# Kernel optimization log

Hardware: AMD Instinct MI355X
Metric: run time of the kernel (lower is better)

The kernel has to match this reference:

```python
import jax, jax.numpy as jnp
import numpy as np

D = 128  # feature_dim

def setup_inputs() -> dict:
    key = jax.random.key(0)
    ks = jax.random.split(key, 10)
    B, Sq, Skv = 32, 2048, 2048
    scale = 1.0 / np.sqrt(D)
    inp = {
        'smiles_features': jax.random.normal(ks[0], (B, Skv, D), jnp.float32),
        'image_features': jax.random.normal(ks[1], (B, Sq, D), jnp.float32),
        'Wv': jax.random.normal(ks[2], (D, D), jnp.float32) * scale,
        'bv': jnp.zeros((D,), jnp.float32),
        'Wk': jax.random.normal(ks[3], (D, D), jnp.float32) * scale,
        'bk': jnp.zeros((D,), jnp.float32),
        'Wq': jax.random.normal(ks[4], (D, D), jnp.float32) * scale,
        'bq': jnp.zeros((D,), jnp.float32),
        'Wd': jax.random.normal(ks[5], (D, D), jnp.float32) * scale,
        'bd': jnp.zeros((D,), jnp.float32),
    }
    return inp

def reference(smiles_features, image_features, Wv, bv, Wk, bk, Wq, bq, Wd, bd):
    # Linear layers: y = x @ W^T + b (torch convention)
    V = smiles_features @ Wv.T + bv          # [B, Skv, D]
    K = smiles_features @ Wk.T + bk          # [B, Skv, D]
    Q = image_features @ Wq.T + bq           # [B, Sq, D]
    # energy = Q K^T / sqrt(128) (hard-coded 128 in original)
    energy = jnp.einsum('bqd,bkd->bqk', Q, K) / jnp.sqrt(jnp.float32(128.0))
    attention = jax.nn.softmax(energy, axis=-1)
    fusion = jnp.einsum('bqk,bkd->bqd', attention, V)
    output = fusion @ Wd.T + bd
    return output
```

## Files before the change

### kernel.cpp

```cpp
#include <hip/hip_runtime.h>
#include <hip/hip_bf16.h>

typedef __attribute__((ext_vector_type(4))) float f32x4;
typedef __attribute__((ext_vector_type(16))) float f32x16;
typedef __attribute__((ext_vector_type(8))) short bf16x8;
typedef __attribute__((ext_vector_type(4))) unsigned int uint4v;
typedef __attribute__((ext_vector_type(2))) unsigned int uint2v;

#define MFMA16(a, b, c) __builtin_amdgcn_mfma_f32_16x16x32_bf16(a, b, c, 0, 0, 0)
#define MFMA32(a, b, c) __builtin_amdgcn_mfma_f32_32x32x16_bf16(a, b, c, 0, 0, 0)

__device__ __forceinline__ unsigned short f2bf(float f) {
  union { float f; unsigned u; } v; v.f = f;
  unsigned r = v.u + 0x7fffu + ((v.u >> 16) & 1u);
  return (unsigned short)(r >> 16);
}
__device__ __forceinline__ unsigned pack2(float a, float b) {
  union { __hip_bfloat162 h2; unsigned u; } cv;
  cv.h2 = __hip_bfloat162(__float2bfloat16(a), __float2bfloat16(b));
  return cv.u;
}

__device__ __forceinline__ void swap32(unsigned a, unsigned b, int hi,
                                       unsigned& ox, unsigned& oy) {
#if __has_builtin(__builtin_amdgcn_permlane32_swap)
  uint2v r = __builtin_amdgcn_permlane32_swap(a, b, false, false);
  ox = r[0]; oy = r[1];
#else
  unsigned sb = __shfl_xor(b, 32);
  unsigned sa = __shfl_xor(a, 32);
  ox = hi ? sb : a;
  oy = hi ? b : sa;
#endif
}

template<bool IN_F32, int OUT_MODE>
__global__ __launch_bounds__(256)
void proj_kernel(const void* __restrict__ xin, const float* __restrict__ W,
                 const float* __restrict__ bias, void* __restrict__ yout,
                 float scale)
{
  __shared__ __align__(16) unsigned short Ws[128][136];
  __shared__ __align__(16) unsigned short Xs[64][136];
  const int t = threadIdx.x;
  const int wid = t >> 6;
  const int lane = t & 63;
  const int ln = lane & 15, g = lane >> 4;
  const long row0 = (long)blockIdx.x * 64;

  float bz[8];
#pragma unroll
  for (int tt = 0; tt < 8; ++tt) bz[tt] = bias[tt * 16 + ln];

#pragma unroll
  for (int i = 0; i < 16; ++i) {
    int idx = (i * 256 + t) * 4;
    int r = idx >> 7, c = idx & 127;
    const float4 w4 = *reinterpret_cast<const float4*>(W + idx);
    ushort4 wb;
    wb.x = f2bf(w4.x); wb.y = f2bf(w4.y); wb.z = f2bf(w4.z); wb.w = f2bf(w4.w);
    *reinterpret_cast<ushort4*>(&Ws[r][c]) = wb;
  }
  if (IN_F32) {
    const float* x = (const float*)xin;
#pragma unroll
    for (int i = 0; i < 8; ++i) {
      int idx = (i * 256 + t) * 4;
      int r = idx >> 7, c = idx & 127;
      const float4 x4 = *reinterpret_cast<const float4*>(x + row0 * 128 + idx);
      ushort4 xb;
      xb.x = f2bf(x4.x); xb.y = f2bf(x4.y); xb.z = f2bf(x4.z); xb.w = f2bf(x4.w);
      *reinterpret_cast<ushort4*>(&Xs[r][c]) = xb;
    }
  } else {
    const unsigned short* x = (const unsigned short*)xin;
#pragma unroll
    for (int i = 0; i < 4; ++i) {
      int idx = (i * 256 + t) * 8;
      int r = idx >> 7, c = idx & 127;
      *reinterpret_cast<uint4v*>(&Xs[r][c]) =
          *reinterpret_cast<const uint4v*>(x + row0 * 128 + idx);
    }
  }
  __syncthreads();

  f32x4 acc[8];
#pragma unroll
  for (int tt = 0; tt < 8; ++tt) acc[tt] = (f32x4){0.f, 0.f, 0.f, 0.f};

#pragma unroll
  for (int c = 0; c < 4; ++c) {
    bf16x8 af = *reinterpret_cast<const bf16x8*>(&Xs[wid * 16 + ln][c * 32 + g * 8]);
#pragma unroll
    for (int tt = 0; tt < 8; ++tt) {
      bf16x8 bfr = *reinterpret_cast<const bf16x8*>(&Ws[tt * 16 + ln][c * 32 + g * 8]);
      acc[tt] = MFMA16(af, bfr, acc[tt]);
    }
  }

#pragma unroll
  for (int tt = 0; tt < 8; ++tt) {
#pragma unroll
    for (int r = 0; r < 4; ++r) {
      long row = row0 + wid * 16 + g * 4 + r;
      int col = tt * 16 + ln;
      float val = (acc[tt][r] + bz[tt]) * scale;
      if (OUT_MODE == 2) {
        ((float*)yout)[row * 128 + col] = val;
      } else if (OUT_MODE == 0) {
        ((unsigned short*)yout)[row * 128 + col] = f2bf(val);
      } else {
        long bb = row >> 11, rr = row & 2047;
        ((unsigned short*)yout)[(bb * 128 + col) * 2048 + rr] = f2bf(val);
      }
    }
  }
}

__global__ __launch_bounds__(256)
void proj_kv_kernel(const float* __restrict__ x,
                    const float* __restrict__ Wk, const float* __restrict__ bk,
                    const float* __restrict__ Wv, const float* __restrict__ bv,
                    unsigned short* __restrict__ Kout,
                    unsigned short* __restrict__ Vout)
{
  __shared__ __align__(16) unsigned short Ws[128][136];
  __shared__ __align__(16) unsigned short Xs[64][136];
  const int t = threadIdx.x;
  const int wid = t >> 6;
  const int lane = t & 63;
  const int ln = lane & 15, g = lane >> 4;
  const long row0 = (long)blockIdx.x * 64;

  float bzk[8], bzv[8];
#pragma unroll
  for (int tt = 0; tt < 8; ++tt) { bzk[tt] = bk[tt * 16 + ln]; bzv[tt] = bv[tt * 16 + ln]; }

#pragma unroll
  for (int i = 0; i < 8; ++i) {
    int idx = (i * 256 + t) * 4;
    int r = idx >> 7, c = idx & 127;
    const float4 x4 = *reinterpret_cast<const float4*>(x + row0 * 128 + idx);
    ushort4 xb;
    xb.x = f2bf(x4.x); xb.y = f2bf(x4.y); xb.z = f2bf(x4.z); xb.w = f2bf(x4.w);
    *reinterpret_cast<ushort4*>(&Xs[r][c]) = xb;
  }
#pragma unroll
  for (int i = 0; i < 16; ++i) {
    int idx = (i * 256 + t) * 4;
    int r = idx >> 7, c = idx & 127;
    const float4 w4 = *reinterpret_cast<const float4*>(Wk + idx);
    ushort4 wb;
    wb.x = f2bf(w4.x); wb.y = f2bf(w4.y); wb.z = f2bf(w4.z); wb.w = f2bf(w4.w);
    *reinterpret_cast<ushort4*>(&Ws[r][c]) = wb;
  }
  __syncthreads();

  f32x4 acc[8];
#pragma unroll
  for (int tt = 0; tt < 8; ++tt) acc[tt] = (f32x4){0.f, 0.f, 0.f, 0.f};
#pragma unroll
  for (int c = 0; c < 4; ++c) {
    bf16x8 af = *reinterpret_cast<const bf16x8*>(&Xs[wid * 16 + ln][c * 32 + g * 8]);
#pragma unroll
    for (int tt = 0; tt < 8; ++tt) {
      bf16x8 bfr = *reinterpret_cast<const bf16x8*>(&Ws[tt * 16 + ln][c * 32 + g * 8]);
      acc[tt] = MFMA16(af, bfr, acc[tt]);
    }
  }
#pragma unroll
  for (int tt = 0; tt < 8; ++tt)
#pragma unroll
    for (int r = 0; r < 4; ++r) {
      long row = row0 + wid * 16 + g * 4 + r;
      Kout[row * 128 + tt * 16 + ln] = f2bf(acc[tt][r] + bzk[tt]);
    }

  __syncthreads();
#pragma unroll
  for (int i = 0; i < 16; ++i) {
    int idx = (i * 256 + t) * 4;
    int r = idx >> 7, c = idx & 127;
    const float4 w4 = *reinterpret_cast<const float4*>(Wv + idx);
    ushort4 wb;
    wb.x = f2bf(w4.x); wb.y = f2bf(w4.y); wb.z = f2bf(w4.z); wb.w = f2bf(w4.w);
    *reinterpret_cast<ushort4*>(&Ws[r][c]) = wb;
  }
  __syncthreads();

#pragma unroll
  for (int tt = 0; tt < 8; ++tt) acc[tt] = (f32x4){0.f, 0.f, 0.f, 0.f};
#pragma unroll
  for (int c = 0; c < 4; ++c) {
    bf16x8 af = *reinterpret_cast<const bf16x8*>(&Xs[wid * 16 + ln][c * 32 + g * 8]);
#pragma unroll
    for (int tt = 0; tt < 8; ++tt) {
      bf16x8 bfr = *reinterpret_cast<const bf16x8*>(&Ws[tt * 16 + ln][c * 32 + g * 8]);
      acc[tt] = MFMA16(af, bfr, acc[tt]);
    }
  }
#pragma unroll
  for (int tt = 0; tt < 8; ++tt)
#pragma unroll
    for (int r = 0; r < 4; ++r) {
      long row = row0 + wid * 16 + g * 4 + r;
      long bb = row >> 11, rr = row & 2047;
      Vout[(bb * 128 + tt * 16 + ln) * 2048 + rr] = f2bf(acc[tt][r] + bzv[tt]);
    }
}

__global__ __launch_bounds__(256)
void attn_kernel(const unsigned short* __restrict__ Qg,
                 const unsigned short* __restrict__ Kg,
                 const unsigned short* __restrict__ Vtg,
                 unsigned short* __restrict__ Fg)
{
  __shared__ __align__(16) unsigned short Ks[32][136];
  __shared__ __align__(16) unsigned short Vs[128][40];

  const int t = threadIdx.x;
  const int lane = t & 63;
  const int q = lane & 31;
  const int hi = lane >> 5;
  const int wid = t >> 6;

  const int gbid = blockIdx.x;
  const int k_ = gbid >> 3, r_ = gbid & 7;
  const int b = r_ + 8 * (k_ >> 4);
  const int j = k_ & 15;
  const int q0 = j * 128 + wid * 32;

  const unsigned short* Qb = Qg + (long)b * 2048 * 128;
  const unsigned short* Kb = Kg + (long)b * 2048 * 128;
  const unsigned short* Vb = Vtg + (long)b * 128 * 2048;

  const int kr = t >> 4, kc = (t & 15) * 8;
  const int vc = t >> 2, ko = (t & 3) * 8;

  bf16x8 qf[8];
#pragma unroll
  for (int c = 0; c < 8; ++c)
    qf[c] = *reinterpret_cast<const bf16x8*>(
        Qb + (long)(q0 + q) * 128 + c * 16 + hi * 8);

  f32x16 o[4];
#pragma unroll
  for (int dc = 0; dc < 4; ++dc)
#pragma unroll
    for (int r = 0; r < 16; ++r) o[dc][r] = 0.f;
  float mrun = -1e30f;
  float lrun = 0.f;

  uint4v kreg0 = *reinterpret_cast<const uint4v*>(Kb + (long)kr * 128 + kc);
  uint4v kreg1 = *reinterpret_cast<const uint4v*>(Kb + (long)(kr + 16) * 128 + kc);
  uint4v vreg0 = *reinterpret_cast<const uint4v*>(Vb + (long)vc * 2048 + ko);
  uint4v vreg1 = *reinterpret_cast<const uint4v*>(Vb + (long)(vc + 64) * 2048 + ko);

  for (int kt = 0; kt < 64; ++kt) {
    __syncthreads();
    *reinterpret_cast<uint4v*>(&Ks[kr][kc]) = kreg0;
    *reinterpret_cast<uint4v*>(&Ks[kr + 16][kc]) = kreg1;
    *reinterpret_cast<uint4v*>(&Vs[vc][ko]) = vreg0;
    *reinterpret_cast<uint4v*>(&Vs[vc + 64][ko]) = vreg1;
    __syncthreads();

    if (kt < 63) {
      const int nv0 = (kt + 1) * 32;
      kreg0 = *reinterpret_cast<const uint4v*>(Kb + (long)(nv0 + kr) * 128 + kc);
      kreg1 = *reinterpret_cast<const uint4v*>(Kb + (long)(nv0 + kr + 16) * 128 + kc);
      vreg0 = *reinterpret_cast<const uint4v*>(Vb + (long)vc * 2048 + nv0 + ko);
      vreg1 = *reinterpret_cast<const uint4v*>(Vb + (long)(vc + 64) * 2048 + nv0 + ko);
    }

    f32x16 st;
#pragma unroll
    for (int r = 0; r < 16; ++r) st[r] = 0.f;
    __builtin_amdgcn_s_setprio(1);
#pragma unroll
    for (int c = 0; c < 8; ++c) {
      bf16x8 kf = *reinterpret_cast<const bf16x8*>(&Ks[q][c * 16 + hi * 8]);
      st = MFMA32(kf, qf[c], st);
    }
    __builtin_amdgcn_s_setprio(0);

    float tm = st[0];
#pragma unroll
    for (int r = 1; r < 16; ++r) tm = fmaxf(tm, st[r]);
    tm = fmaxf(tm, __shfl_xor(tm, 32));

    float mcur = mrun;
    if (!__all(tm <= mcur + 8.0f)) {
      float mnew = fmaxf(mcur, tm);
      float al = __builtin_amdgcn_exp2f(mcur - mnew);
      mrun = mnew;
      mcur = mnew;
      lrun *= al;
#pragma unroll
      for (int r = 0; r < 16; ++r) {
        float ar = __shfl(al, (r & 3) + 8 * (r >> 2) + 4 * hi);
#pragma unroll
        for (int dc = 0; dc < 4; ++dc) o[dc][r] *= ar;
      }
    }

    unsigned pk[8];
    float s[8];
#pragma unroll
    for (int j2 = 0; j2 < 8; ++j2) {
      float pa_ = __builtin_amdgcn_exp2f(st[2 * j2] - mcur);
      float pb_ = __builtin_amdgcn_exp2f(st[2 * j2 + 1] - mcur);
      s[j2] = pa_ + pb_;
      pk[j2] = pack2(pa_, pb_);
    }
#pragma unroll
    for (int j2 = 0; j2 < 4; ++j2) s[j2] += s[j2 + 4];
    lrun += (s[0] + s[1]) + (s[2] + s[3]);

    union { unsigned u[4]; bf16x8 v; } pa0, pa1;
    swap32(pk[0], pk[2], hi, pa0.u[0], pa0.u[2]);
    swap32(pk[1], pk[3], hi, pa0.u[1], pa0.u[3]);
    swap32(pk[4], pk[6], hi, pa1.u[0], pa1.u[2]);
    swap32(pk[5], pk[7], hi, pa1.u[1], pa1.u[3]);

    __builtin_amdgcn_s_setprio(1);
#pragma unroll
    for (int dc = 0; dc < 4; ++dc) {
      bf16x8 vf0 = *reinterpret_cast<const bf16x8*>(&Vs[dc * 32 + q][hi * 8]);
      bf16x8 vf1 = *reinterpret_cast<const bf16x8*>(&Vs[dc * 32 + q][16 + hi * 8]);
      o[dc] = MFMA32(pa0.v, vf0, o[dc]);
      o[dc] = MFMA32(pa1.v, vf1, o[dc]);
    }
    __builtin_amdgcn_s_setprio(0);
  }

  float ltot = lrun + __shfl_xor(lrun, 32);
  float inv = 1.f / ltot;
#pragma unroll
  for (int r = 0; r < 16; ++r) {
    const int qr = (r & 3) + 8 * (r >> 2) + 4 * hi;
    float invr = __shfl(inv, qr);
    long row = (long)b * 2048 + q0 + qr;
#pragma unroll
    for (int dc = 0; dc < 4; ++dc)
      Fg[row * 128 + dc * 32 + q] = f2bf(o[dc][r] * invr);
  }
}

extern "C" void kernel_launch(void* const* d_in, const int* in_sizes, int n_in,
                              void* d_out, int out_size, void* d_ws, size_t ws_size,
                              hipStream_t stream)
{
  (void)in_sizes; (void)n_in; (void)out_size; (void)ws_size;
  const float* smiles = (const float*)d_in[0];
  const float* image  = (const float*)d_in[1];
  const float* Wv = (const float*)d_in[2]; const float* bv = (const float*)d_in[3];
  const float* Wk = (const float*)d_in[4]; const float* bk = (const float*)d_in[5];
  const float* Wq = (const float*)d_in[6]; const float* bq = (const float*)d_in[7];
  const float* Wd = (const float*)d_in[8]; const float* bd = (const float*)d_in[9];

  unsigned short* Qw = (unsigned short*)d_ws;
  unsigned short* Kw = Qw + 8388608;
  unsigned short* Vw = Kw + 8388608;
  unsigned short* Fw = Vw + 8388608;

  const float qscale = 1.4426950408889634f * 0.08838834764831845f;

  dim3 blk(256);
  proj_kernel<true, 0><<<dim3(1024), blk, 0, stream>>>(image, Wq, bq, Qw, qscale);
  proj_kv_kernel<<<dim3(1024), blk, 0, stream>>>(smiles, Wk, bk, Wv, bv, Kw, Vw);
  attn_kernel<<<dim3(512), blk, 0, stream>>>(Qw, Kw, Vw, Fw);
  proj_kernel<false, 2><<<dim3(1024), blk, 0, stream>>>(Fw, Wd, bd, (float*)d_out, 1.f);
}
```

Measured before the change: 128.1 us.

## Process two 32-row query tiles per wave to reuse K/V LDS fragments

Each wave now handles 64 query rows (two 32-row tiles) instead of 32, so every K and V fragment read from shared memory feeds two MFMAs and each block covers 256 query rows. The grid shrinks from 512 to 256 blocks, halving the global K/V tile traffic per query and the sync overhead per unit of work. The cost is roughly doubled accumulator and Q register usage, which may lower occupancy. With only 256 blocks, the grid may also underfill the GPU's 256 CUs.

```diff
diff --git a/kernel.cpp b/kernel.cpp
--- a/kernel.cpp
+++ b/kernel.cpp
@@ -226,9 +226,9 @@
 
   const int gbid = blockIdx.x;
   const int k_ = gbid >> 3, r_ = gbid & 7;
-  const int b = r_ + 8 * (k_ >> 4);
-  const int j = k_ & 15;
-  const int q0 = j * 128 + wid * 32;
+  const int b = r_ + 8 * (k_ >> 3);
+  const int j = k_ & 7;
+  const int q0 = j * 256 + wid * 64;
 
   const unsigned short* Qb = Qg + (long)b * 2048 * 128;
   const unsigned short* Kb = Kg + (long)b * 2048 * 128;
@@ -237,19 +237,60 @@
   const int kr = t >> 4, kc = (t & 15) * 8;
   const int vc = t >> 2, ko = (t & 3) * 8;
 
-  bf16x8 qf[8];
-#pragma unroll
-  for (int c = 0; c < 8; ++c)
-    qf[c] = *reinterpret_cast<const bf16x8*>(
+  bf16x8 qf0[8], qf1[8];
+#pragma unroll
+  for (int c = 0; c < 8; ++c) {
+    qf0[c] = *reinterpret_cast<const bf16x8*>(
         Qb + (long)(q0 + q) * 128 + c * 16 + hi * 8);
-
-  f32x16 o[4];
+    qf1[c] = *reinterpret_cast<const bf16x8*>(
+        Qb + (long)(q0 + 32 + q) * 128 + c * 16 + hi * 8);
+  }
+
+  f32x16 o0[4], o1[4];
 #pragma unroll
   for (int dc = 0; dc < 4; ++dc)
 #pragma unroll
-    for (int r = 0; r < 16; ++r) o[dc][r] = 0.f;
-  float mrun = -1e30f;
-  float lrun = 0.f;
+    for (int r = 0; r < 16; ++r) { o0[dc][r] = 0.f; o1[dc][r] = 0.f; }
+  float mrun0 = -1e30f, mrun1 = -1e30f;
+  float lrun0 = 0.f, lrun1 = 0.f;
+
+  auto softmax_fn = [&](const f32x16& st, float& mr, float& lr, f32x16* oacc,
+                        bf16x8& pav0, bf16x8& pav1) {
+    float tm = st[0];
+#pragma unroll
+    for (int r = 1; r < 16; ++r) tm = fmaxf(tm, st[r]);
+    tm = fmaxf(tm, __shfl_xor(tm, 32));
+    float mcur = mr;
+    if (!__all(tm <= mcur + 8.0f)) {
+      float mnew = fmaxf(mcur, tm);
+      float al = __builtin_amdgcn_exp2f(mcur - mnew);
+      mr = mnew; mcur = mnew; lr *= al;
+#pragma unroll
+      for (int r = 0; r < 16; ++r) {
+        float ar = __shfl(al, (r & 3) + 8 * (r >> 2) + 4 * hi);
+#pragma unroll
+        for (int dc = 0; dc < 4; ++dc) oacc[dc][r] *= ar;
+      }
+    }
+    unsigned pk[8];
+    float s[8];
+#pragma unroll
+    for (int j2 = 0; j2 < 8; ++j2) {
+      float pa_ = __builtin_amdgcn_exp2f(st[2 * j2] - mcur);
+      float pb_ = __builtin_amdgcn_exp2f(st[2 * j2 + 1] - mcur);
+      s[j2] = pa_ + pb_;
+      pk[j2] = pack2(pa_, pb_);
+    }
+#pragma unroll
+    for (int j2 = 0; j2 < 4; ++j2) s[j2] += s[j2 + 4];
+    lr += (s[0] + s[1]) + (s[2] + s[3]);
+    union { unsigned u[4]; bf16x8 v; } A, B;
+    swap32(pk[0], pk[2], hi, A.u[0], A.u[2]);
+    swap32(pk[1], pk[3], hi, A.u[1], A.u[3]);
+    swap32(pk[4], pk[6], hi, B.u[0], B.u[2]);
+    swap32(pk[5], pk[7], hi, B.u[1], B.u[3]);
+    pav0 = A.v; pav1 = B.v;
+  };
 
   uint4v kreg0 = *reinterpret_cast<const uint4v*>(Kb + (long)kr * 128 + kc);
   uint4v kreg1 = *reinterpret_cast<const uint4v*>(Kb + (long)(kr + 16) * 128 + kc);
@@ -272,77 +313,60 @@
       vreg1 = *reinterpret_cast<const uint4v*>(Vb + (long)(vc + 64) * 2048 + nv0 + ko);
     }
 
-    f32x16 st;
-#pragma unroll
-    for (int r = 0; r < 16; ++r) st[r] = 0.f;
+    f32x16 st0, st1;
+#pragma unroll
+    for (int r = 0; r < 16; ++r) { st0[r] = 0.f; st1[r] = 0.f; }
     __builtin_amdgcn_s_setprio(1);
 #pragma unroll
     for (int c = 0; c < 8; ++c) {
       bf16x8 kf = *reinterpret_cast<const bf16x8*>(&Ks[q][c * 16 + hi * 8]);
-      st = MFMA32(kf, qf[c], st);
+      st0 = MFMA32(kf, qf0[c], st0);
+      st1 = MFMA32(kf, qf1[c], st1);
     }
     __builtin_amdgcn_s_setprio(0);
 
-    float tm = st[0];
-#pragma unroll
-    for (int r = 1; r < 16; ++r) tm = fmaxf(tm, st[r]);
-    tm = fmaxf(tm, __shfl_xor(tm, 32));
-
-    float mcur = mrun;
-    if (!__all(tm <= mcur + 8.0f)) {
-      float mnew = fmaxf(mcur, tm);
-      float al = __builtin_amdgcn_exp2f(mcur - mnew);
-      mrun = mnew;
-      mcur = mnew;
-      lrun *= al;
-#pragma unroll
-      for (int r = 0; r < 16; ++r) {
-        float ar = __shfl(al, (r & 3) + 8 * (r >> 2) + 4 * hi);
-#pragma unroll
-        for (int dc = 0; dc < 4; ++dc) o[dc][r] *= ar;
-      }
-    }
-
-    unsigned pk[8];
-    float s[8];
-#pragma unroll
-    for (int j2 = 0; j2 < 8; ++j2) {
-      float pa_ = __builtin_amdgcn_exp2f(st[2 * j2] - mcur);
-      float pb_ = __builtin_amdgcn_exp2f(st[2 * j2 + 1] - mcur);
-      s[j2] = pa_ + pb_;
-      pk[j2] = pack2(pa_, pb_);
-    }
-#pragma unroll
-    for (int j2 = 0; j2 < 4; ++j2) s[j2] += s[j2 + 4];
-    lrun += (s[0] + s[1]) + (s[2] + s[3]);
-
-    union { unsigned u[4]; bf16x8 v; } pa0, pa1;
-    swap32(pk[0], pk[2], hi, pa0.u[0], pa0.u[2]);
-    swap32(pk[1], pk[3], hi, pa0.u[1], pa0.u[3]);
-    swap32(pk[4], pk[6], hi, pa1.u[0], pa1.u[2]);
-    swap32(pk[5], pk[7], hi, pa1.u[1], pa1.u[3]);
+    bf16x8 paA0, paA1, paB0, paB1;
+    softmax_fn(st0, mrun0, lrun0, o0, paA0, paA1);
+    softmax_fn(st1, mrun1, lrun1, o1, paB0, paB1);
 
     __builtin_amdgcn_s_setprio(1);
 #pragma unroll
     for (int dc = 0; dc < 4; ++dc) {
       bf16x8 vf0 = *reinterpret_cast<const bf16x8*>(&Vs[dc * 32 + q][hi * 8]);
       bf16x8 vf1 = *reinterpret_cast<const bf16x8*>(&Vs[dc * 32 + q][16 + hi * 8]);
-      o[dc] = MFMA32(pa0.v, vf0, o[dc]);
-      o[dc] = MFMA32(pa1.v, vf1, o[dc]);
+      o0[dc] = MFMA32(paA0, vf0, o0[dc]);
+      o0[dc] = MFMA32(paA1, vf1, o0[dc]);
+      o1[dc] = MFMA32(paB0, vf0, o1[dc]);
+      o1[dc] = MFMA32(paB1, vf1, o1[dc]);
     }
     __builtin_amdgcn_s_setprio(0);
   }
 
-  float ltot = lrun + __shfl_xor(lrun, 32);
-  float inv = 1.f / ltot;
-#pragma unroll
-  for (int r = 0; r < 16; ++r) {
-    const int qr = (r & 3) + 8 * (r >> 2) + 4 * hi;
-    float invr = __shfl(inv, qr);
-    long row = (long)b * 2048 + q0 + qr;
-#pragma unroll
-    for (int dc = 0; dc < 4; ++dc)
-      Fg[row * 128 + dc * 32 + q] = f2bf(o[dc][r] * invr);
+  {
+    float ltot = lrun0 + __shfl_xor(lrun0, 32);
+    float inv = 1.f / ltot;
+#pragma unroll
+    for (int r = 0; r < 16; ++r) {
+      const int qr = (r & 3) + 8 * (r >> 2) + 4 * hi;
+      float invr = __shfl(inv, qr);
+      long row = (long)b * 2048 + q0 + qr;
+#pragma unroll
+      for (int dc = 0; dc < 4; ++dc)
+        Fg[row * 128 + dc * 32 + q] = f2bf(o0[dc][r] * invr);
+    }
+  }
+  {
+    float ltot = lrun1 + __shfl_xor(lrun1, 32);
+    float inv = 1.f / ltot;
+#pragma unroll
+    for (int r = 0; r < 16; ++r) {
+      const int qr = (r & 3) + 8 * (r >> 2) + 4 * hi;
+      float invr = __shfl(inv, qr);
+      long row = (long)b * 2048 + q0 + 32 + qr;
+#pragma unroll
+      for (int dc = 0; dc < 4; ++dc)
+        Fg[row * 128 + dc * 32 + q] = f2bf(o1[dc][r] * invr);
+    }
   }
 }
 
@@ -368,6 +392,6 @@
   dim3 blk(256);
   proj_kernel<true, 0><<<dim3(1024), blk, 0, stream>>>(image, Wq, bq, Qw, qscale);
   proj_kv_kernel<<<dim3(1024), blk, 0, stream>>>(smiles, Wk, bk, Wv, bv, Kw, Vw);
-  attn_kernel<<<dim3(512), blk, 0, stream>>>(Qw, Kw, Vw, Fw);
+  attn_kernel<<<dim3(256), blk, 0, stream>>>(Qw, Kw, Vw, Fw);
   proj_kernel<false, 2><<<dim3(1024), blk, 0, stream>>>(Fw, Wd, bd, (float*)d_out, 1.f);
 }
```

After: 170.2 us. +32.9%, slower.

## Merge Q/KV projections into one launch and double-buffer attention K/V tiles

Applied to the files above, without the earlier changes.

The Q projection and the K/V projection become one kernel with 2048 blocks, where the block index selects Q or K/V work. This removes one launch and lets both run concurrently on the GPU. The attention kernel now double-buffers its K and V shared-memory tiles, keeping one barrier per iteration instead of two and prefetching two tiles ahead. The cost is more LDS per block, which could lower occupancy, and uneven work between Q blocks and KV blocks in the merged launch.

```diff
diff --git a/kernel.cpp b/kernel.cpp
--- a/kernel.cpp
+++ b/kernel.cpp
@@ -107,22 +107,23 @@
       float val = (acc[tt][r] + bz[tt]) * scale;
       if (OUT_MODE == 2) {
         ((float*)yout)[row * 128 + col] = val;
-      } else if (OUT_MODE == 0) {
+      } else {
         ((unsigned short*)yout)[row * 128 + col] = f2bf(val);
-      } else {
-        long bb = row >> 11, rr = row & 2047;
-        ((unsigned short*)yout)[(bb * 128 + col) * 2048 + rr] = f2bf(val);
       }
     }
   }
 }
 
 __global__ __launch_bounds__(256)
-void proj_kv_kernel(const float* __restrict__ x,
-                    const float* __restrict__ Wk, const float* __restrict__ bk,
-                    const float* __restrict__ Wv, const float* __restrict__ bv,
-                    unsigned short* __restrict__ Kout,
-                    unsigned short* __restrict__ Vout)
+void proj_qkv_kernel(const float* __restrict__ image,
+                     const float* __restrict__ Wq, const float* __restrict__ bq,
+                     float qscale,
+                     const float* __restrict__ smiles,
+                     const float* __restrict__ Wk, const float* __restrict__ bk,
+                     const float* __restrict__ Wv, const float* __restrict__ bv,
+                     unsigned short* __restrict__ Qout,
+                     unsigned short* __restrict__ Kout,
+                     unsigned short* __restrict__ Vout)
 {
   __shared__ __align__(16) unsigned short Ws[128][136];
   __shared__ __align__(16) unsigned short Xs[64][136];
@@ -130,11 +131,9 @@
   const int wid = t >> 6;
   const int lane = t & 63;
   const int ln = lane & 15, g = lane >> 4;
-  const long row0 = (long)blockIdx.x * 64;
-
-  float bzk[8], bzv[8];
-#pragma unroll
-  for (int tt = 0; tt < 8; ++tt) { bzk[tt] = bk[tt * 16 + ln]; bzv[tt] = bv[tt * 16 + ln]; }
+  const bool isQ = blockIdx.x < 1024;
+  const long row0 = (long)(isQ ? blockIdx.x : blockIdx.x - 1024) * 64;
+  const float* x = isQ ? image : smiles;
 
 #pragma unroll
   for (int i = 0; i < 8; ++i) {
@@ -145,11 +144,18 @@
     xb.x = f2bf(x4.x); xb.y = f2bf(x4.y); xb.z = f2bf(x4.z); xb.w = f2bf(x4.w);
     *reinterpret_cast<ushort4*>(&Xs[r][c]) = xb;
   }
+
+  const float* W1 = isQ ? Wq : Wk;
+  const float* b1 = isQ ? bq : bk;
+  float bz[8];
+#pragma unroll
+  for (int tt = 0; tt < 8; ++tt) bz[tt] = b1[tt * 16 + ln];
+
 #pragma unroll
   for (int i = 0; i < 16; ++i) {
     int idx = (i * 256 + t) * 4;
     int r = idx >> 7, c = idx & 127;
-    const float4 w4 = *reinterpret_cast<const float4*>(Wk + idx);
+    const float4 w4 = *reinterpret_cast<const float4*>(W1 + idx);
     ushort4 wb;
     wb.x = f2bf(w4.x); wb.y = f2bf(w4.y); wb.z = f2bf(w4.z); wb.w = f2bf(w4.w);
     *reinterpret_cast<ushort4*>(&Ws[r][c]) = wb;
@@ -168,12 +174,24 @@
       acc[tt] = MFMA16(af, bfr, acc[tt]);
     }
   }
+
+  if (isQ) {
+#pragma unroll
+    for (int tt = 0; tt < 8; ++tt)
+#pragma unroll
+      for (int r = 0; r < 4; ++r) {
+        long row = row0 + wid * 16 + g * 4 + r;
+        Qout[row * 128 + tt * 16 + ln] = f2bf((acc[tt][r] + bz[tt]) * qscale);
+      }
+    return;
+  }
+
 #pragma unroll
   for (int tt = 0; tt < 8; ++tt)
 #pragma unroll
     for (int r = 0; r < 4; ++r) {
       long row = row0 + wid * 16 + g * 4 + r;
-      Kout[row * 128 + tt * 16 + ln] = f2bf(acc[tt][r] + bzk[tt]);
+      Kout[row * 128 + tt * 16 + ln] = f2bf(acc[tt][r] + bz[tt]);
     }
 
   __syncthreads();
@@ -188,6 +206,9 @@
   }
   __syncthreads();
 
+  float bzv[8];
+#pragma unroll
+  for (int tt = 0; tt < 8; ++tt) bzv[tt] = bv[tt * 16 + ln];
 #pragma unroll
   for (int tt = 0; tt < 8; ++tt) acc[tt] = (f32x4){0.f, 0.f, 0.f, 0.f};
 #pragma unroll
@@ -215,8 +236,8 @@
                  const unsigned short* __restrict__ Vtg,
                  unsigned short* __restrict__ Fg)
 {
-  __shared__ __align__(16) unsigned short Ks[32][136];
-  __shared__ __align__(16) unsigned short Vs[128][40];
+  __shared__ __align__(16) unsigned short Ks[2][32][136];
+  __shared__ __align__(16) unsigned short Vs[2][128][40];
 
   const int t = threadIdx.x;
   const int lane = t & 63;
@@ -255,21 +276,32 @@
   uint4v kreg1 = *reinterpret_cast<const uint4v*>(Kb + (long)(kr + 16) * 128 + kc);
   uint4v vreg0 = *reinterpret_cast<const uint4v*>(Vb + (long)vc * 2048 + ko);
   uint4v vreg1 = *reinterpret_cast<const uint4v*>(Vb + (long)(vc + 64) * 2048 + ko);
+  *reinterpret_cast<uint4v*>(&Ks[0][kr][kc]) = kreg0;
+  *reinterpret_cast<uint4v*>(&Ks[0][kr + 16][kc]) = kreg1;
+  *reinterpret_cast<uint4v*>(&Vs[0][vc][ko]) = vreg0;
+  *reinterpret_cast<uint4v*>(&Vs[0][vc + 64][ko]) = vreg1;
+  kreg0 = *reinterpret_cast<const uint4v*>(Kb + (long)(32 + kr) * 128 + kc);
+  kreg1 = *reinterpret_cast<const uint4v*>(Kb + (long)(32 + kr + 16) * 128 + kc);
+  vreg0 = *reinterpret_cast<const uint4v*>(Vb + (long)vc * 2048 + 32 + ko);
+  vreg1 = *reinterpret_cast<const uint4v*>(Vb + (long)(vc + 64) * 2048 + 32 + ko);
+  __syncthreads();
 
   for (int kt = 0; kt < 64; ++kt) {
-    __syncthreads();
-    *reinterpret_cast<uint4v*>(&Ks[kr][kc]) = kreg0;
-    *reinterpret_cast<uint4v*>(&Ks[kr + 16][kc]) = kreg1;
-    *reinterpret_cast<uint4v*>(&Vs[vc][ko]) = vreg0;
-    *reinterpret_cast<uint4v*>(&Vs[vc + 64][ko]) = vreg1;
-    __syncthreads();
+    const int cur = kt & 1;
 
     if (kt < 63) {
-      const int nv0 = (kt + 1) * 32;
-      kreg0 = *reinterpret_cast<const uint4v*>(Kb + (long)(nv0 + kr) * 128 + kc);
-      kreg1 = *reinterpret_cast<const uint4v*>(Kb + (long)(nv0 + kr + 16) * 128 + kc);
-      vreg0 = *reinterpret_cast<const uint4v*>(Vb + (long)vc * 2048 + nv0 + ko);
-      vreg1 = *reinterpret_cast<const uint4v*>(Vb + (long)(vc + 64) * 2048 + nv0 + ko);
+      const int nb = cur ^ 1;
+      *reinterpret_cast<uint4v*>(&Ks[nb][kr][kc]) = kreg0;
+      *reinterpret_cast<uint4v*>(&Ks[nb][kr + 16][kc]) = kreg1;
+      *reinterpret_cast<uint4v*>(&Vs[nb][vc][ko]) = vreg0;
+      *reinterpret_cast<uint4v*>(&Vs[nb][vc + 64][ko]) = vreg1;
+      if (kt < 62) {
+        const int nv0 = (kt + 2) * 32;
+        kreg0 = *reinterpret_cast<const uint4v*>(Kb + (long)(nv0 + kr) * 128 + kc);
+        kreg1 = *reinterpret_cast<const uint4v*>(Kb + (long)(nv0 + kr + 16) * 128 + kc);
+        vreg0 = *reinterpret_cast<const uint4v*>(Vb + (long)vc * 2048 + nv0 + ko);
+        vreg1 = *reinterpret_cast<const uint4v*>(Vb + (long)(vc + 64) * 2048 + nv0 + ko);
+      }
     }
 
     f32x16 st;
@@ -278,7 +310,7 @@
     __builtin_amdgcn_s_setprio(1);
 #pragma unroll
     for (int c = 0; c < 8; ++c) {
-      bf16x8 kf = *reinterpret_cast<const bf16x8*>(&Ks[q][c * 16 + hi * 8]);
+      bf16x8 kf = *reinterpret_cast<const bf16x8*>(&Ks[cur][q][c * 16 + hi * 8]);
       st = MFMA32(kf, qf[c], st);
     }
     __builtin_amdgcn_s_setprio(0);
@@ -325,12 +357,14 @@
     __builtin_amdgcn_s_setprio(1);
 #pragma unroll
     for (int dc = 0; dc < 4; ++dc) {
-      bf16x8 vf0 = *reinterpret_cast<const bf16x8*>(&Vs[dc * 32 + q][hi * 8]);
-      bf16x8 vf1 = *reinterpret_cast<const bf16x8*>(&Vs[dc * 32 + q][16 + hi * 8]);
+      bf16x8 vf0 = *reinterpret_cast<const bf16x8*>(&Vs[cur][dc * 32 + q][hi * 8]);
+      bf16x8 vf1 = *reinterpret_cast<const bf16x8*>(&Vs[cur][dc * 32 + q][16 + hi * 8]);
       o[dc] = MFMA32(pa0.v, vf0, o[dc]);
       o[dc] = MFMA32(pa1.v, vf1, o[dc]);
     }
     __builtin_amdgcn_s_setprio(0);
+
+    __syncthreads();
   }
 
   float ltot = lrun + __shfl_xor(lrun, 32);
@@ -366,8 +400,9 @@
   const float qscale = 1.4426950408889634f * 0.08838834764831845f;
 
   dim3 blk(256);
-  proj_kernel<true, 0><<<dim3(1024), blk, 0, stream>>>(image, Wq, bq, Qw, qscale);
-  proj_kv_kernel<<<dim3(1024), blk, 0, stream>>>(smiles, Wk, bk, Wv, bv, Kw, Vw);
+  proj_qkv_kernel<<<dim3(2048), blk, 0, stream>>>(image, Wq, bq, qscale,
+                                                  smiles, Wk, bk, Wv, bv,
+                                                  Qw, Kw, Vw);
   attn_kernel<<<dim3(512), blk, 0, stream>>>(Qw, Kw, Vw, Fw);
   proj_kernel<false, 2><<<dim3(1024), blk, 0, stream>>>(Fw, Wd, bd, (float*)d_out, 1.f);
 }
```

Result: no change. 126.0 us (-1.6%).
